# Kernel tuning notes

Measured on AMD Instinct MI355X. Metric: run time of the kernel, lower is better.

## Reference

```python
import jax, jax.numpy as jnp
import numpy as np

B, T, C, H, D = 8, 2048, 1024, 1024, 4  # batch, seq_len, input_size, hidden_size, dilation


def setup_inputs() -> dict:
    key = jax.random.key(0)
    k1, k2, k3, k4, k5 = jax.random.split(key, 5)
    s = 1.0 / np.sqrt(H).astype(np.float32)  # match nn.LSTM uniform(-1/sqrt(H),1/sqrt(H)) scale
    return {
        "x": jax.random.normal(k1, (B, T, C), jnp.float32),
        "W_ih": jax.random.normal(k2, (4 * H, C), jnp.float32) * s,
        "W_hh": jax.random.normal(k3, (4 * H, H), jnp.float32) * s,
        "b_ih": jax.random.normal(k4, (4 * H,), jnp.float32) * s,
        "b_hh": jax.random.normal(k5, (4 * H,), jnp.float32) * s,
    }


def _dilated_lstm(x, W_ih, W_hh, b_ih, b_hh):
    Bv, Tv, Cv = x.shape
    Tp = -(-Tv // D) * D          # ceil(T/D)*D, static
    L = Tp // D                   # sub-sequence length per dilation phase
    xp = jnp.pad(x, ((0, 0), (0, Tp - Tv), (0, 0)))
    # (B, L, D, C) -> (B, D, L, C) -> (B*D, L, C): D parallel strided slices
    xr = xp.reshape(Bv, L, D, Cv).transpose(0, 2, 1, 3).reshape(Bv * D, L, Cv)
    # Precompute input contribution to all gates once (big GEMM, hoisted out of scan)
    xg = jnp.einsum('blc,gc->blg', xr, W_ih) + b_ih + b_hh  # (B*D, L, 4H)

    h0 = jnp.zeros((Bv * D, H), x.dtype)
    c0 = jnp.zeros((Bv * D, H), x.dtype)

    def step(carry, g_t):
        h, c = carry
        g = g_t + h @ W_hh.T                    # (B*D, 4H), torch gate order i,f,g,o
        i, f, gg, o = jnp.split(g, 4, axis=-1)
        i = jax.nn.sigmoid(i)
        f = jax.nn.sigmoid(f)
        gg = jnp.tanh(gg)
        o = jax.nn.sigmoid(o)
        c = f * c + i * gg
        h = o * jnp.tanh(c)
        return (h, c), h

    _, ys = jax.lax.scan(step, (h0, c0), xg.transpose(1, 0, 2))  # ys: (L, B*D, H)
    y = ys.transpose(1, 0, 2)                                    # (B*D, L, H)
    y = y.reshape(Bv, D, L, H).transpose(0, 2, 1, 3).reshape(Bv, Tp, H)
    return y[:, :Tv, :]


def reference(x, W_ih, W_hh, b_ih, b_hh):
    return _dilated_lstm(x, W_ih, W_hh, b_ih, b_hh)
```

## Files before the change

kernel.cpp:

```cpp
#include <hip/hip_runtime.h>
#include <cstdint>

typedef __attribute__((ext_vector_type(8))) _Float16 half8;
typedef __attribute__((ext_vector_type(4))) _Float16 half4;
typedef __attribute__((ext_vector_type(4))) float f32x4;
typedef unsigned short u16;
typedef unsigned int u32;
typedef unsigned long long u64;

#define MFMA16F(a, b, c) __builtin_amdgcn_mfma_f32_16x16x32_f16((a), (b), (c), 0, 0, 0)
#define AGENT __HIP_MEMORY_SCOPE_AGENT

__device__ __forceinline__ void gl_lds16_coh(const void* g, void* lds) {
  __builtin_amdgcn_global_load_lds(
      (const __attribute__((address_space(1))) unsigned*)g,
      (__attribute__((address_space(3))) unsigned*)lds, 16, 0, 17);
}
__device__ __forceinline__ void gl_lds16(const void* g, void* lds) {
  __builtin_amdgcn_global_load_lds(
      (const __attribute__((address_space(1))) unsigned*)g,
      (__attribute__((address_space(3))) unsigned*)lds, 16, 0, 0);
}

__device__ __forceinline__ float sigm(float x) { return 1.f / (1.f + __expf(-x)); }
__device__ __forceinline__ float tanh_f(float x) { return 2.f / (1.f + __expf(-2.f * x)) - 1.f; }

__global__ void k_cvt(const float* __restrict__ in, _Float16* __restrict__ o, int n4) {
  int i = blockIdx.x * blockDim.x + threadIdx.x;
  int stride = gridDim.x * blockDim.x;
  for (; i < n4; i += stride) {
    float4 v = ((const float4*)in)[i];
    half4 h = {(_Float16)v.x, (_Float16)v.y, (_Float16)v.z, (_Float16)v.w};
    ((half4*)o)[i] = h;
  }
}

__global__ void k_bias(const float* __restrict__ bi, const float* __restrict__ bh,
                       float* __restrict__ bias) {
  int i = blockIdx.x * blockDim.x + threadIdx.x;
  if (i < 4096) bias[i] = bi[i] + bh[i];
}

__global__ void k_init4(u64* __restrict__ hf) {
  const int i = blockIdx.x * blockDim.x + threadIdx.x;
  const u64 v = (i < 8192) ? 0ull : 0x0001000100010001ull;
  __hip_atomic_store(&hf[i], v, __ATOMIC_RELAXED, AGENT);
}

__global__ __launch_bounds__(256) void k_gemm1(
    const u16* __restrict__ Aw, const u16* __restrict__ Bw,
    const float* __restrict__ bias, _Float16* __restrict__ xg) {
  __shared__ u16 sA[4096];
  __shared__ u16 sB[4096];
  const int tid = threadIdx.x, lane = tid & 63, wid = tid >> 6;
  const int bm = blockIdx.x >> 5, bn = blockIdx.x & 31;
  const int m0 = bm * 128, n0 = bn * 128;
  const int wr = wid >> 1, wc = wid & 1;
  f32x4 acc[4][4] = {};

  for (int kt = 0; kt < 32; ++kt) {
#pragma unroll
    for (int rb = 0; rb < 2; ++rb) {
      const int base = (rb * 4 + wid) * 1024;
      const int b = base + lane * 16;
      const int row = b >> 6;
      const int q = lane & 3;
      const int sq = ((q - row) & 3) << 4;
      gl_lds16((const char*)Aw + (size_t)(m0 + row) * 2048 + (size_t)kt * 64 + sq,
               (char*)&sA[0] + base);
      gl_lds16((const char*)Bw + (size_t)(n0 + row) * 2048 + (size_t)kt * 64 + sq,
               (char*)&sB[0] + base);
    }
    __syncthreads();
    half8 ah[4], bh[4];
#pragma unroll
    for (int i = 0; i < 4; ++i) {
      const int ra = wr * 64 + i * 16 + (lane & 15);
      ah[i] = *(const half8*)((const char*)sA + ra * 64 + ((((lane >> 4) + ra) & 3) << 4));
      const int rb2 = wc * 64 + i * 16 + (lane & 15);
      bh[i] = *(const half8*)((const char*)sB + rb2 * 64 + ((((lane >> 4) + rb2) & 3) << 4));
    }
#pragma unroll
    for (int i = 0; i < 4; ++i)
#pragma unroll
      for (int j = 0; j < 4; ++j) acc[i][j] = MFMA16F(ah[i], bh[j], acc[i][j]);
    __syncthreads();
  }

#pragma unroll
  for (int j = 0; j < 4; ++j) {
    const int gcol = n0 + wc * 64 + j * 16 + (lane & 15);
    const int gate = gcol >> 10, jj = gcol & 1023;
    const float bv = bias[gcol];
#pragma unroll
    for (int i = 0; i < 4; ++i)
#pragma unroll
      for (int q = 0; q < 4; ++q) {
        const int m = m0 + wr * 64 + i * 16 + (lane >> 4) * 4 + q;
        const int b = m >> 11, t = m & 2047;
        const int s = (b << 2) | (t & 3);
        const int l = t >> 2;
        xg[(((size_t)(l * 32 + s)) * 1024 + jj) * 4 + gate] = (_Float16)(acc[i][j][q] + bv);
      }
  }
}

__global__ __launch_bounds__(512, 1) void k_scan(
    const u16* __restrict__ Whh16, const _Float16* __restrict__ xg,
    u16* __restrict__ hfrag, float* __restrict__ out) {
  __shared__ u16 h_lds[2][8192];
  const int tid = threadIdx.x;
  const int lane = tid & 63, wid = tid >> 6;
  const int w = blockIdx.x;
  const int gr = w >> 5;
  const int wl = w & 31;
  const int j0 = wl * 32;

  half8 wf[32];
  {
    const int p = lane & 15;
    const int gate = p >> 2, c = p & 3;
    const int koff = (lane >> 4) * 8;
    const size_t rowbase = (size_t)(gate * 1024 + j0 + wid * 4 + c) * 1024;
#pragma unroll
    for (int ks = 0; ks < 32; ++ks) {
      wf[ks] = *(const half8*)(Whh16 + rowbase + ks * 32 + koff);
      asm volatile("" : "+v"(wf[ks]));
    }
  }

  const int m = ((lane >> 4) << 2) | ((lane >> 2) & 3);
  const int jl = (wid << 2) | (lane & 3);
  const int s = gr * 8 + m;
  const int j = j0 + jl;
  float c_reg = 0.f;
  const int hq = wl * 64 + (wid >> 1) * 16 + m * 2 + (wid & 1);

  const u64 M = 0x0001000100010001ull;

  float x0 = 0.f, x1 = 0.f, x2 = 0.f, x3 = 0.f;
  if (lane < 32) {
    const half4 xv = *(const half4*)(xg + ((size_t)s * 1024 + j) * 4);
    x0 = (float)xv[0]; x1 = (float)xv[1]; x2 = (float)xv[2]; x3 = (float)xv[3];
  }

  for (int l = 0; l < 512; ++l) {
    const char* hsrc = (const char*)hfrag + (size_t)(l & 3) * 65536 + gr * 16384;
    u64* hdst = (u64*)((char*)hfrag + (size_t)((l + 1) & 3) * 65536 + gr * 16384);
    const u64 expv = ((l >> 2) & 1) ? M : 0ull;
    const u32 pw = (u32)(((l + 1) >> 2) & 1);
    u16* ldsb = &h_lds[l & 1][0];

    for (;;) {
#pragma unroll
      for (int r = 0; r < 2; ++r)
        gl_lds16_coh(hsrc + wid * 2048 + r * 1024 + lane * 16,
                     (char*)ldsb + wid * 2048 + r * 1024);
      asm volatile("s_waitcnt vmcnt(0)" ::: "memory");
      bool ok = true;
#pragma unroll
      for (int r = 0; r < 2; ++r) {
        const u64* q = (const u64*)((const char*)ldsb + wid * 2048 + r * 1024 + lane * 16);
        ok = ok & (((q[0] ^ expv) & M) == 0) & (((q[1] ^ expv) & M) == 0);
      }
      if (__all(ok)) break;
    }
    __syncthreads();

    f32x4 a0 = {0.f, 0.f, 0.f, 0.f}, a1 = a0, a2 = a0, a3 = a0;
    const char* ab = (const char*)ldsb + (lane >> 4) * 128 + (lane & 7) * 16;
#pragma unroll
    for (int ks = 0; ks < 32; ks += 4) {
      const char* cb = ab + ks * 512;
      a0 = MFMA16F(*(const half8*)(cb), wf[ks], a0);
      a1 = MFMA16F(*(const half8*)(cb + 512), wf[ks + 1], a1);
      a2 = MFMA16F(*(const half8*)(cb + 1024), wf[ks + 2], a2);
      a3 = MFMA16F(*(const half8*)(cb + 1536), wf[ks + 3], a3);
    }
    float G0 = (a0[0] + a1[0]) + (a2[0] + a3[0]);
    float G1 = (a0[1] + a1[1]) + (a2[1] + a3[1]);
    float G2 = (a0[2] + a1[2]) + (a2[2] + a3[2]);
    float G3 = (a0[3] + a1[3]) + (a2[3] + a3[3]);

    {
      const bool h2 = (lane & 4) != 0;
      float x, y;
      x = h2 ? G0 : G1; y = __shfl_xor(x, 4);
      G0 = h2 ? y : G0; G1 = h2 ? G1 : y;
      x = h2 ? G2 : G3; y = __shfl_xor(x, 4);
      G2 = h2 ? y : G2; G3 = h2 ? G3 : y;
    }
    {
      const bool h3 = (lane & 8) != 0;
      float x, y;
      x = h3 ? G0 : G2; y = __shfl_xor(x, 8);
      G0 = h3 ? y : G0; G2 = h3 ? G2 : y;
      x = h3 ? G1 : G3; y = __shfl_xor(x, 8);
      G1 = h3 ? y : G1; G3 = h3 ? G3 : y;
    }

    const float gi = G0 + x0, gf = G1 + x1, gg = G2 + x2, go = G3 + x3;
    const float iv = sigm(gi), fv = sigm(gf), gv = tanh_f(gg), ov = sigm(go);
    c_reg = fv * c_reg + iv * gv;
    const float hv = ov * tanh_f(c_reg);

    if (lane < 32) {
      u32 hb = (u32)__builtin_bit_cast(u16, (_Float16)hv);
      hb = (hb & 0xFFFEu) | pw;
      const u32 o1 = (u32)__shfl_xor((int)hb, 1);
      const u32 w1 = (lane & 1) ? ((o1 & 0xFFFFu) | (hb << 16))
                                : ((hb & 0xFFFFu) | (o1 << 16));
      const u32 o2lo = (u32)__shfl_xor((int)w1, 2);
      const u64 v = (lane & 2) ? (((u64)w1 << 32) | (u64)o2lo)
                               : (((u64)o2lo << 32) | (u64)w1);
      if ((lane & 3) == 0)
        __hip_atomic_store(&hdst[hq], v, __ATOMIC_RELAXED, AGENT);

      out[(((size_t)(s >> 2) * 2048) + (size_t)l * 4 + (s & 3)) * 1024 + j] = hv;

      if (l < 511) {
        const half4 xv = *(const half4*)(xg + (((size_t)(l + 1) * 32 + s) * 1024 + j) * 4);
        x0 = (float)xv[0]; x1 = (float)xv[1]; x2 = (float)xv[2]; x3 = (float)xv[3];
      }
    }
  }
}

extern "C" void kernel_launch(void* const* d_in, const int* in_sizes, int n_in,
                              void* d_out, int out_size, void* d_ws, size_t ws_size,
                              hipStream_t stream) {
  const float* x   = (const float*)d_in[0];
  const float* Wih = (const float*)d_in[1];
  const float* Whh = (const float*)d_in[2];
  const float* bih = (const float*)d_in[3];
  const float* bhh = (const float*)d_in[4];
  float* out = (float*)d_out;
  char* ws = (char*)d_ws;

  constexpr size_t OFF_WIH16 = 0;
  constexpr size_t OFF_WHH16 = 8388608;
  constexpr size_t OFF_BIAS  = 16777216;
  constexpr size_t OFF_HFRAG = 16793600;
  constexpr size_t OFF_XG    = 17055744;
  constexpr size_t WS_NEED   = OFF_XG + 134217728;

  if (ws_size < WS_NEED) {
    hipMemsetAsync(d_out, 0, (size_t)out_size * sizeof(float), stream);
    return;
  }

  _Float16* wih16 = (_Float16*)(ws + OFF_WIH16);
  _Float16* whh16 = (_Float16*)(ws + OFF_WHH16);
  float* bias = (float*)(ws + OFF_BIAS);
  u16* hfrag = (u16*)(ws + OFF_HFRAG);
  _Float16* xg = (_Float16*)(ws + OFF_XG);
  _Float16* x16 = (_Float16*)d_out;

  k_cvt<<<1024, 256, 0, stream>>>(Wih, wih16, 4194304 / 4);
  k_cvt<<<1024, 256, 0, stream>>>(Whh, whh16, 4194304 / 4);
  k_cvt<<<2048, 256, 0, stream>>>(x, x16, 16777216 / 4);
  k_bias<<<16, 256, 0, stream>>>(bih, bhh, bias);
  k_init4<<<128, 256, 0, stream>>>((u64*)hfrag);
  k_gemm1<<<4096, 256, 0, stream>>>((const u16*)x16, (const u16*)wih16, bias, xg);
  k_scan<<<128, 512, 0, stream>>>((const u16*)whh16, xg, hfrag, out);
}
```

Baseline: 1.267 ms.

## Remap scan blocks for XCD locality and poll h with cheaper cache policy

The scan kernel now launches 256 blocks and lets only those with blockIdx&7 < 4 do work, so each recurrence group's blocks land on a fixed subset of XCDs under round-robin dispatch. The spin-wait on the hidden-state buffer first polls with a lighter cache-policy flag (aux=1) and falls back to the fully coherent policy (aux=17) after 64 failed tries. The aim is to cut cross-die latency on the per-step handoff between blocks. It relies on undocumented block-to-XCD placement, and the lighter poll may keep reading stale cached data, which costs extra spins before the fallback kicks in.

```diff
diff --git a/kernel.cpp b/kernel.cpp
--- a/kernel.cpp
+++ b/kernel.cpp
@@ -11,15 +11,11 @@
 #define MFMA16F(a, b, c) __builtin_amdgcn_mfma_f32_16x16x32_f16((a), (b), (c), 0, 0, 0)
 #define AGENT __HIP_MEMORY_SCOPE_AGENT
 
-__device__ __forceinline__ void gl_lds16_coh(const void* g, void* lds) {
+template <int AUX>
+__device__ __forceinline__ void gl_lds16_a(const void* g, void* lds) {
   __builtin_amdgcn_global_load_lds(
       (const __attribute__((address_space(1))) unsigned*)g,
-      (__attribute__((address_space(3))) unsigned*)lds, 16, 0, 17);
-}
-__device__ __forceinline__ void gl_lds16(const void* g, void* lds) {
-  __builtin_amdgcn_global_load_lds(
-      (const __attribute__((address_space(1))) unsigned*)g,
-      (__attribute__((address_space(3))) unsigned*)lds, 16, 0, 0);
+      (__attribute__((address_space(3))) unsigned*)lds, 16, 0, AUX);
 }
 
 __device__ __forceinline__ float sigm(float x) { return 1.f / (1.f + __expf(-x)); }
@@ -66,10 +62,10 @@
       const int row = b >> 6;
       const int q = lane & 3;
       const int sq = ((q - row) & 3) << 4;
-      gl_lds16((const char*)Aw + (size_t)(m0 + row) * 2048 + (size_t)kt * 64 + sq,
-               (char*)&sA[0] + base);
-      gl_lds16((const char*)Bw + (size_t)(n0 + row) * 2048 + (size_t)kt * 64 + sq,
-               (char*)&sB[0] + base);
+      gl_lds16_a<0>((const char*)Aw + (size_t)(m0 + row) * 2048 + (size_t)kt * 64 + sq,
+                    (char*)&sA[0] + base);
+      gl_lds16_a<0>((const char*)Bw + (size_t)(n0 + row) * 2048 + (size_t)kt * 64 + sq,
+                    (char*)&sB[0] + base);
     }
     __syncthreads();
     half8 ah[4], bh[4];
@@ -108,12 +104,14 @@
 __global__ __launch_bounds__(512, 1) void k_scan(
     const u16* __restrict__ Whh16, const _Float16* __restrict__ xg,
     u16* __restrict__ hfrag, float* __restrict__ out) {
+  const int b = blockIdx.x;
+  const int gr = b & 7;
+  if (gr >= 4) return;
+  const int wl = b >> 3;
+  const int tid = threadIdx.x;
+
   __shared__ u16 h_lds[2][8192];
-  const int tid = threadIdx.x;
   const int lane = tid & 63, wid = tid >> 6;
-  const int w = blockIdx.x;
-  const int gr = w >> 5;
-  const int wl = w & 31;
   const int j0 = wl * 32;
 
   half8 wf[32];
@@ -137,6 +135,7 @@
   const int hq = wl * 64 + (wid >> 1) * 16 + m * 2 + (wid & 1);
 
   const u64 M = 0x0001000100010001ull;
+  int mode = 0;
 
   float x0 = 0.f, x1 = 0.f, x2 = 0.f, x3 = 0.f;
   if (lane < 32) {
@@ -151,19 +150,30 @@
     const u32 pw = (u32)(((l + 1) >> 2) & 1);
     u16* ldsb = &h_lds[l & 1][0];
 
-    for (;;) {
-#pragma unroll
-      for (int r = 0; r < 2; ++r)
-        gl_lds16_coh(hsrc + wid * 2048 + r * 1024 + lane * 16,
-                     (char*)ldsb + wid * 2048 + r * 1024);
-      asm volatile("s_waitcnt vmcnt(0)" ::: "memory");
-      bool ok = true;
-#pragma unroll
-      for (int r = 0; r < 2; ++r) {
-        const u64* q = (const u64*)((const char*)ldsb + wid * 2048 + r * 1024 + lane * 16);
-        ok = ok & (((q[0] ^ expv) & M) == 0) & (((q[1] ^ expv) & M) == 0);
+    {
+      int tries = 0;
+      for (;;) {
+        if (mode == 0) {
+#pragma unroll
+          for (int r = 0; r < 2; ++r)
+            gl_lds16_a<1>(hsrc + wid * 2048 + r * 1024 + lane * 16,
+                          (char*)ldsb + wid * 2048 + r * 1024);
+        } else {
+#pragma unroll
+          for (int r = 0; r < 2; ++r)
+            gl_lds16_a<17>(hsrc + wid * 2048 + r * 1024 + lane * 16,
+                           (char*)ldsb + wid * 2048 + r * 1024);
+        }
+        asm volatile("s_waitcnt vmcnt(0)" ::: "memory");
+        bool ok = true;
+#pragma unroll
+        for (int r = 0; r < 2; ++r) {
+          const u64* q = (const u64*)((const char*)ldsb + wid * 2048 + r * 1024 + lane * 16);
+          ok = ok & (((q[0] ^ expv) & M) == 0) & (((q[1] ^ expv) & M) == 0);
+        }
+        if (__all(ok)) break;
+        if (++tries > 64) mode = 1;
       }
-      if (__all(ok)) break;
     }
     __syncthreads();
 
@@ -262,5 +272,5 @@
   k_bias<<<16, 256, 0, stream>>>(bih, bhh, bias);
   k_init4<<<128, 256, 0, stream>>>((u64*)hfrag);
   k_gemm1<<<4096, 256, 0, stream>>>((const u16*)x16, (const u16*)wih16, bias, xg);
-  k_scan<<<128, 512, 0, stream>>>((const u16*)whh16, xg, hfrag, out);
-}
+  k_scan<<<256, 512, 0, stream>>>((const u16*)whh16, xg, hfrag, out);
+}
```

Result: no change. 1.280 ms (+1.0%).
